# Kernel optimization log

Hardware: AMD Instinct MI355X
Metric: run time of the kernel (lower is better)

The kernel has to match this reference:

```python
import jax, jax.numpy as jnp
import numpy as np

D_MODEL = 2048
N_HEADS = 16
N_KV_HEADS = 4
HEAD_DIM = D_MODEL // N_HEADS  # 128
ROPE_BASE = 10000.0


def _rope_tables(T, head_dim):
    half = head_dim // 2
    theta = 1.0 / (ROPE_BASE ** (jnp.arange(half, dtype=jnp.float32) / half))
    m = jnp.arange(T, dtype=jnp.float32)
    freqs = jnp.outer(m, theta)  # (T, half)
    return jnp.cos(freqs), jnp.sin(freqs)


def _apply_rope(x, cos, sin):
    # x: (B, H, T, hd); rotate first/second halves as pairs
    half = x.shape[-1] // 2
    x1, x2 = x[..., :half], x[..., half:]
    cos = cos[None, None, :, :]
    sin = sin[None, None, :, :]
    return jnp.concatenate([x1 * cos - x2 * sin, x1 * sin + x2 * cos], axis=-1)


def setup_inputs() -> dict:
    key = jax.random.key(0)
    ks = jax.random.split(key, 5)
    B, T = 4, 2048
    x = jax.random.normal(ks[0], (B, T, D_MODEL), dtype=jnp.float32)
    Wq = jax.random.normal(ks[1], (D_MODEL, N_HEADS * HEAD_DIM), dtype=jnp.float32) * 0.02
    Wk = jax.random.normal(ks[2], (D_MODEL, N_KV_HEADS * HEAD_DIM), dtype=jnp.float32) * 0.02
    Wv = jax.random.normal(ks[3], (D_MODEL, N_KV_HEADS * HEAD_DIM), dtype=jnp.float32) * 0.02
    Wo = jax.random.normal(ks[4], (N_HEADS * HEAD_DIM, D_MODEL), dtype=jnp.float32) * (0.02 / np.sqrt(2.0))
    return {"x": x, "Wq": Wq, "Wk": Wk, "Wv": Wv, "Wo": Wo}


def reference(x, Wq, Wk, Wv, Wo):
    B, T, C = x.shape
    groups = N_HEADS // N_KV_HEADS

    # QKV projections
    q = (x @ Wq).reshape(B, T, N_HEADS, HEAD_DIM).transpose(0, 2, 1, 3)      # (B,H,T,hd)
    k = (x @ Wk).reshape(B, T, N_KV_HEADS, HEAD_DIM).transpose(0, 2, 1, 3)   # (B,Hkv,T,hd)
    v = (x @ Wv).reshape(B, T, N_KV_HEADS, HEAD_DIM).transpose(0, 2, 1, 3)

    # RoPE on q and k
    cos, sin = _rope_tables(T, HEAD_DIM)
    q = _apply_rope(q, cos, sin)
    k = _apply_rope(k, cos, sin)

    # GQA: repeat each kv head `groups` times
    k = jnp.repeat(k, groups, axis=1)  # (B,H,T,hd)
    v = jnp.repeat(v, groups, axis=1)

    # Attention scores with ALiBi bias and causal mask
    scale = 1.0 / np.sqrt(HEAD_DIM)
    scores = jnp.einsum('bhqd,bhkd->bhqk', q, k) * scale  # (B,H,T,T)

    pos = jnp.arange(T)
    dist = jnp.minimum(pos[None, :] - pos[:, None], 0).astype(jnp.float32)  # (T,T), <=0
    slopes = 2.0 ** (-8.0 * jnp.arange(1, N_HEADS + 1, dtype=jnp.float32) / N_HEADS)
    alibi = slopes[:, None, None] * dist[None, :, :]  # (H,T,T)
    scores = scores + alibi[None]

    causal = pos[None, :] > pos[:, None]  # True = future = blocked
    scores = jnp.where(causal[None, None], -jnp.inf, scores)

    weights = jax.nn.softmax(scores, axis=-1)
    out = jnp.einsum('bhqk,bhkd->bhqd', weights, v)  # (B,H,T,hd)
    out = out.transpose(0, 2, 1, 3).reshape(B, T, N_HEADS * HEAD_DIM)
    return out @ Wo
```

## Files before the change

### kernel.cpp

```cpp
#include <hip/hip_runtime.h>
#include <hip/hip_bf16.h>
#include <stdint.h>

#define T_SEQ 2048
#define DM    2048
#define NH    16
#define NKVH  4
#define HD    128
#define NBATCH 4
#define BT    (NBATCH * T_SEQ)
#define ATT_SCALE 0.08838834764831845f
#define LOG2E 1.4426950408889634f

typedef __attribute__((ext_vector_type(8))) short bf16x8;
typedef __attribute__((ext_vector_type(4))) float f32x4;
typedef __attribute__((ext_vector_type(16))) float f32x16;
typedef __attribute__((ext_vector_type(8))) unsigned short ushort8;
typedef __attribute__((ext_vector_type(4))) unsigned short ushort4v;

static __device__ __forceinline__ unsigned short f2bf(float f) {
  __hip_bfloat16 h = __float2bfloat16(f);
  return __builtin_bit_cast(unsigned short, h);
}
static __device__ __forceinline__ float bf2f(unsigned short u) {
  unsigned int v = ((unsigned int)u) << 16;
  return __builtin_bit_cast(float, v);
}
static __device__ __forceinline__ unsigned int packbf2(float a, float b) {
  return (unsigned int)f2bf(a) | ((unsigned int)f2bf(b) << 16);
}

#define GLDS16(g, l)                                                        \
  __builtin_amdgcn_global_load_lds(                                         \
      (const __attribute__((address_space(1))) void*)(g),                   \
      (__attribute__((address_space(3))) void*)(l), 16, 0, 0)

__global__ __launch_bounds__(256) void castx_k(const float* __restrict__ x,
                                               unsigned short* __restrict__ xb) {
  int i = (blockIdx.x * 256 + threadIdx.x) * 4;
  float4 v = *(const float4*)&x[i];
  ushort4v o;
  o[0] = f2bf(v.x); o[1] = f2bf(v.y); o[2] = f2bf(v.z); o[3] = f2bf(v.w);
  *(ushort4v*)&xb[i] = o;
}

__global__ __launch_bounds__(256) void transw_k(const float* __restrict__ src,
                                                unsigned short* __restrict__ dst,
                                                int ncols) {
  __shared__ unsigned short t[64][72];
  int n0 = blockIdx.x * 64, r0 = blockIdx.y * 64;
  int tid = threadIdx.x;
  int tx = tid & 15, ty = tid >> 4;
#pragma unroll
  for (int i = 0; i < 4; i++) {
    int r = ty * 4 + i;
    float4 v = *(const float4*)&src[(size_t)(r0 + r) * ncols + n0 + tx * 4];
    t[r][tx * 4 + 0] = f2bf(v.x);
    t[r][tx * 4 + 1] = f2bf(v.y);
    t[r][tx * 4 + 2] = f2bf(v.z);
    t[r][tx * 4 + 3] = f2bf(v.w);
  }
  __syncthreads();
  int nl = tid >> 2, seg = tid & 3;
  ushort8 o0, o1;
#pragma unroll
  for (int j = 0; j < 8; j++) {
    o0[j] = t[seg * 16 + j][nl];
    o1[j] = t[seg * 16 + 8 + j][nl];
  }
  size_t base = (size_t)(n0 + nl) * 2048 + r0 + seg * 16;
  *(ushort8*)&dst[base] = o0;
  *(ushort8*)&dst[base + 8] = o1;
}

template <int EPI>
__global__ __launch_bounds__(256) void gemm_k(const unsigned short* __restrict__ A,
                                              const unsigned short* __restrict__ Bt,
                                              unsigned short* __restrict__ q_out,
                                              unsigned short* __restrict__ k_out,
                                              unsigned short* __restrict__ v_out,
                                              float* __restrict__ f_out) {
  __shared__ unsigned short As[128 * 32];
  __shared__ unsigned short Bs[128 * 32];
  const int tid = threadIdx.x;
  const int lane = tid & 63;
  const int wid = tid >> 6;
  const int wr = wid >> 1, wc = wid & 1;
  const int row0 = blockIdx.x * 128, n00 = blockIdx.y * 128;
  const int lr = lane & 15, lk = (lane >> 4) * 8;
  const int c0 = tid, c1 = tid + 256;

  f32x4 acc[4][4] = {};

  for (int k0 = 0; k0 < 2048; k0 += 32) {
    __syncthreads();
    GLDS16(A + (size_t)(row0 + (c0 >> 2)) * 2048 + k0 + (c0 & 3) * 8, &As[c0 * 8]);
    GLDS16(A + (size_t)(row0 + (c1 >> 2)) * 2048 + k0 + (c1 & 3) * 8, &As[c1 * 8]);
    GLDS16(Bt + (size_t)(n00 + (c0 >> 2)) * 2048 + k0 + (c0 & 3) * 8, &Bs[c0 * 8]);
    GLDS16(Bt + (size_t)(n00 + (c1 >> 2)) * 2048 + k0 + (c1 & 3) * 8, &Bs[c1 * 8]);
    __syncthreads();
    bf16x8 af[4], bfr[4];
#pragma unroll
    for (int mi = 0; mi < 4; mi++)
      af[mi] = *(const bf16x8*)&As[(wr * 64 + mi * 16 + lr) * 32 + lk];
#pragma unroll
    for (int ni = 0; ni < 4; ni++)
      bfr[ni] = *(const bf16x8*)&Bs[(wc * 64 + ni * 16 + lr) * 32 + lk];
#pragma unroll
    for (int mi = 0; mi < 4; mi++)
#pragma unroll
      for (int ni = 0; ni < 4; ni++)
        acc[mi][ni] =
            __builtin_amdgcn_mfma_f32_16x16x32_bf16(af[mi], bfr[ni], acc[mi][ni], 0, 0, 0);
  }

  const int rbase = row0 + wr * 64;
  const int cbase = n00 + wc * 64;
#pragma unroll
  for (int mi = 0; mi < 4; mi++)
#pragma unroll
    for (int ni = 0; ni < 4; ni++)
#pragma unroll
      for (int r = 0; r < 4; r++) {
        int row = rbase + mi * 16 + (lane >> 4) * 4 + r;
        int col = cbase + ni * 16 + lr;
        float v = acc[mi][ni][r];
        if (EPI == 0) {
          if (col < 2048) {
            q_out[(size_t)row * 2048 + col] = f2bf(v);
          } else if (col < 2560) {
            k_out[(size_t)row * 512 + (col - 2048)] = f2bf(v);
          } else {
            int nv = col - 2560;
            int kvh = nv >> 7, d = nv & 127;
            int b = row >> 11, tt = row & 2047;
            v_out[((size_t)(b * NKVH + kvh) * HD + d) * T_SEQ + tt] = f2bf(v);
          }
        } else {
          f_out[(size_t)row * 2048 + col] = v;
        }
      }
}

__global__ __launch_bounds__(256) void rope_k(unsigned short* __restrict__ qb,
                                              unsigned short* __restrict__ kb) {
  int idx = blockIdx.x * 256 + threadIdx.x;
  int i = idx & 63;
  int wi = idx >> 6;
  int hh = wi % (NH + NKVH);
  int bt = wi / (NH + NKVH);
  int t = bt & (T_SEQ - 1);
  unsigned short* p = (hh < NH) ? (qb + (size_t)bt * 2048 + hh * HD)
                                : (kb + (size_t)bt * 512 + (hh - NH) * HD);
  float theta = exp2f(-(float)i * (13.287712379549449f / 64.0f));
  float ang = (float)t * theta;
  float s, c;
  sincosf(ang, &s, &c);
  float x1 = bf2f(p[i]), x2 = bf2f(p[i + 64]);
  p[i] = f2bf(x1 * c - x2 * s);
  p[i + 64] = f2bf(x1 * s + x2 * c);
}

__global__ __launch_bounds__(256) void attn_k(const unsigned short* __restrict__ qb,
                                              const unsigned short* __restrict__ kb,
                                              const unsigned short* __restrict__ vt,
                                              unsigned short* __restrict__ ao) {
  __shared__ __align__(16) unsigned short smem[17408];

  const int bid = blockIdx.x;
  const int level = bid >> 6;
  const int j = 15 - level;
  const int rr = bid & 63;
  const int s8 = rr & 7;
  const int w8 = rr >> 3;
  const int g = s8 + 8 * (w8 & 1);
  const int hh = w8 >> 1;
  const int b = g >> 2, kvh = g & 3;
  const int h = kvh * 4 + hh;

  const int tid = threadIdx.x;
  const int wid = tid >> 6, lane = tid & 63;
  const int l31 = lane & 31, lh = lane >> 5;
  const float slope2 = exp2f(-0.5f * (float)(h + 1)) * LOG2E;
  const float scale2 = ATT_SCALE * LOG2E;

  const int q0 = j * 128 + wid * 32;
  const int dt_w = j * 4 + wid;
  const int T_blk = j * 4 + 4;

  const int krow = tid >> 4;
  const int kchunk = tid & 15;
  const int cgk = kchunk ^ (krow & 7);
  const int vrow = tid >> 2;
  const int vchunk = tid & 3;
  const int cgv = vchunk ^ (vrow & 3);
  const int kxor = l31 & 7;
  const int vxor = l31 & 3;

  const unsigned short* khead = kb + (size_t)(b * T_SEQ) * 512 + kvh * 128;
  const unsigned short* vhead = vt + (size_t)(b * NKVH + kvh) * HD * T_SEQ;

  auto stage = [&](int buf, int k0) {
#pragma unroll
    for (int c = 0; c < 2; c++)
      GLDS16(khead + (size_t)(k0 + c * 16 + krow) * 512 + cgk * 8,
             &smem[buf * 4096 + c * 2048 + tid * 8]);
#pragma unroll
    for (int c = 0; c < 2; c++)
      GLDS16(vhead + (size_t)(c * 64 + vrow) * T_SEQ + k0 + cgv * 8,
             &smem[8192 + buf * 4096 + c * 2048 + tid * 8]);
  };

  unsigned short (*ot)[32][136] = (unsigned short(*)[32][136])smem;

  const unsigned short* qrow =
      qb + ((size_t)(b * T_SEQ + q0 + l31)) * 2048 + h * HD + lh * 8;
  bf16x8 qf[8];
#pragma unroll
  for (int ds = 0; ds < 8; ds++) qf[ds] = *(const bf16x8*)&qrow[ds * 16];

  f32x16 oacc[4] = {};
  float m2 = -1e30f, l_sum = 0.f;
  const float arow = -slope2 * (float)(q0 + l31);

  stage(0, 32 * (T_blk - 1));
  __syncthreads();
  int cur = 0;

#pragma unroll 1
  for (int it = 0; it < T_blk; ++it) {
    const int tt = T_blk - 1 - it;
    if (it + 1 < T_blk) stage(cur ^ 1, 32 * (tt - 1));

    if (tt <= dt_w) {
      const int k0 = tt * 32;
      const unsigned short* Kb = &smem[cur * 4096];
      const unsigned short* Vb = &smem[8192 + cur * 4096];

      bf16x8 kf[8];
#pragma unroll
      for (int ds = 0; ds < 8; ds++)
        kf[ds] = *(const bf16x8*)&Kb[l31 * 128 + ((2 * ds + lh) ^ kxor) * 8];

      __builtin_amdgcn_s_setprio(1);
      f32x16 sca = 0.f, scb = 0.f;
#pragma unroll
      for (int ds = 0; ds < 4; ds++)
        sca = __builtin_amdgcn_mfma_f32_32x32x16_bf16(kf[ds], qf[ds], sca, 0, 0, 0);
#pragma unroll
      for (int ds = 4; ds < 8; ds++)
        scb = __builtin_amdgcn_mfma_f32_32x32x16_bf16(kf[ds], qf[ds], scb, 0, 0, 0);
      __builtin_amdgcn_s_setprio(0);

      bf16x8 vf[4][2];
#pragma unroll
      for (int dt = 0; dt < 4; dt++)
#pragma unroll
        for (int ks = 0; ks < 2; ks++)
          vf[dt][ks] =
              *(const bf16x8*)&Vb[(dt * 32 + l31) * 32 + ((2 * ks + lh) ^ vxor) * 8];

      float s[16];
      const float ab = fmaf(slope2, (float)k0, arow);
      const bool diag = (tt == dt_w);
#pragma unroll
      for (int r = 0; r < 16; r++) {
        const int crow = (r & 3) + 8 * (r >> 2) + 4 * lh;
        float v = fmaf(sca[r] + scb[r], scale2, fmaf(slope2, (float)crow, ab));
        if (diag && crow > l31) v = -1e30f;
        s[r] = v;
      }

      float t8[8], t4[4];
#pragma unroll
      for (int i = 0; i < 8; i++) t8[i] = fmaxf(s[i], s[i + 8]);
#pragma unroll
      for (int i = 0; i < 4; i++) t4[i] = fmaxf(t8[i], t8[i + 4]);
      float mx = fmaxf(fmaxf(t4[0], t4[1]), fmaxf(t4[2], t4[3]));
      mx = fmaxf(mx, __shfl_xor(mx, 32));

      if (__any(mx > m2 + 8.f)) {
        const float mnew = fmaxf(m2, mx);
        const float corr = exp2f(m2 - mnew);
        l_sum *= corr;
#pragma unroll
        for (int dt = 0; dt < 4; dt++) oacc[dt] *= corr;
        m2 = mnew;
      }

      float pr[16];
#pragma unroll
      for (int r = 0; r < 16; r++) pr[r] = exp2f(s[r] - m2);

      float a8[8], a4[4];
#pragma unroll
      for (int i = 0; i < 8; i++) a8[i] = pr[i] + pr[i + 8];
#pragma unroll
      for (int i = 0; i < 4; i++) a4[i] = a8[i] + a8[i + 4];
      float rs = (a4[0] + a4[1]) + (a4[2] + a4[3]);
      rs += __shfl_xor(rs, 32);
      l_sum += rs;

      unsigned int w[8];
#pragma unroll
      for (int i = 0; i < 8; i++) w[i] = packbf2(pr[2 * i], pr[2 * i + 1]);
      const unsigned int ta = __shfl_xor(lh ? w[0] : w[2], 32);
      const unsigned int tb = __shfl_xor(lh ? w[1] : w[3], 32);
      const unsigned int tc = __shfl_xor(lh ? w[4] : w[6], 32);
      const unsigned int td = __shfl_xor(lh ? w[5] : w[7], 32);
      union U4 { unsigned int u[4]; bf16x8 v; } f0, f1;
      f0.u[0] = lh ? ta : w[0];
      f0.u[1] = lh ? tb : w[1];
      f0.u[2] = lh ? w[2] : ta;
      f0.u[3] = lh ? w[3] : tb;
      f1.u[0] = lh ? tc : w[4];
      f1.u[1] = lh ? td : w[5];
      f1.u[2] = lh ? w[6] : tc;
      f1.u[3] = lh ? w[7] : td;

      __builtin_amdgcn_s_setprio(1);
#pragma unroll
      for (int dt = 0; dt < 4; dt++) {
        oacc[dt] =
            __builtin_amdgcn_mfma_f32_32x32x16_bf16(vf[dt][0], f0.v, oacc[dt], 0, 0, 0);
        oacc[dt] =
            __builtin_amdgcn_mfma_f32_32x32x16_bf16(vf[dt][1], f1.v, oacc[dt], 0, 0, 0);
      }
      __builtin_amdgcn_s_setprio(0);
    }

    __syncthreads();
    cur ^= 1;
  }

  const float inv = 1.0f / l_sum;
#pragma unroll
  for (int dt = 0; dt < 4; dt++)
#pragma unroll
    for (int rg = 0; rg < 4; rg++) {
      ushort4v o;
#pragma unroll
      for (int jj = 0; jj < 4; jj++) o[jj] = f2bf(oacc[dt][rg * 4 + jj] * inv);
      *(ushort4v*)&ot[wid][l31][dt * 32 + rg * 8 + lh * 4] = o;
    }
  __syncthreads();
  const int rrow = lane >> 4, chunk = lane & 15;
#pragma unroll
  for (int ps = 0; ps < 8; ps++) {
    const int row = ps * 4 + rrow;
    ushort8 v = *(const ushort8*)&ot[wid][row][chunk * 8];
    *(ushort8*)&ao[((size_t)(b * T_SEQ + q0 + row)) * 2048 + h * HD + chunk * 8] = v;
  }
}

extern "C" void kernel_launch(void* const* d_in, const int* in_sizes, int n_in,
                              void* d_out, int out_size, void* d_ws, size_t ws_size,
                              hipStream_t stream) {
  const float* x = (const float*)d_in[0];
  const float* Wq = (const float*)d_in[1];
  const float* Wk = (const float*)d_in[2];
  const float* Wv = (const float*)d_in[3];
  const float* Wo = (const float*)d_in[4];

  char* w = (char*)d_ws;
  unsigned short* xb = (unsigned short*)w;
  unsigned short* wqt = (unsigned short*)(w + 33554432);
  unsigned short* qb = (unsigned short*)(w + 33554432 + 12582912);
  unsigned short* kb = (unsigned short*)(w + 33554432 + 12582912 + 33554432);
  unsigned short* vtb = (unsigned short*)(w + 33554432 + 12582912 + 33554432 + 8388608);

  castx_k<<<16384, 256, 0, stream>>>(x, xb);
  transw_k<<<dim3(32, 32), 256, 0, stream>>>(Wq, wqt, 2048);
  transw_k<<<dim3(8, 32), 256, 0, stream>>>(Wk, wqt + (size_t)2048 * 2048, 512);
  transw_k<<<dim3(8, 32), 256, 0, stream>>>(Wv, wqt + (size_t)2560 * 2048, 512);
  gemm_k<0><<<dim3(64, 24), 256, 0, stream>>>(xb, wqt, qb, kb, vtb, nullptr);
  rope_k<<<40960, 256, 0, stream>>>(qb, kb);
  transw_k<<<dim3(32, 32), 256, 0, stream>>>(Wo, wqt, 2048);
  attn_k<<<1024, 256, 0, stream>>>(qb, kb, vtb, xb);
  gemm_k<1><<<dim3(64, 16), 256, 0, stream>>>(xb, wqt, nullptr, nullptr, nullptr,
                                              (float*)d_out);
}
```

Measured before the change: 486.7 us.

## Pair causal query tiles per block and stage 64-key tiles in attention

Each attention block now handles two query tiles, j and 15-j, one after the other, so every block does the same causal work. The grid drops from 1024 to 512 blocks. K/V staging moves from 32-key to 64-key tiles, which doubles shared memory to 64KB and halves the number of barrier iterations. This targets load imbalance and the tail from the causal triangle. In exchange it lowers occupancy, since larger LDS per block may allow fewer resident blocks, and it serializes the two halves within each block.

```diff
diff --git a/kernel.cpp b/kernel.cpp
--- a/kernel.cpp
+++ b/kernel.cpp
@@ -165,16 +165,14 @@
                                               const unsigned short* __restrict__ kb,
                                               const unsigned short* __restrict__ vt,
                                               unsigned short* __restrict__ ao) {
-  __shared__ __align__(16) unsigned short smem[17408];
+  __shared__ __align__(16) unsigned short smem[32768];
 
   const int bid = blockIdx.x;
-  const int level = bid >> 6;
-  const int j = 15 - level;
-  const int rr = bid & 63;
-  const int s8 = rr & 7;
-  const int w8 = rr >> 3;
-  const int g = s8 + 8 * (w8 & 1);
-  const int hh = w8 >> 1;
+  const int s8 = bid & 7;
+  const int rest = bid >> 3;
+  const int p = rest & 7;
+  const int hh = (rest >> 3) & 3;
+  const int g = s8 + 8 * (rest >> 5);
   const int b = g >> 2, kvh = g & 3;
   const int h = kvh * 4 + hh;
 
@@ -184,172 +182,176 @@
   const float slope2 = exp2f(-0.5f * (float)(h + 1)) * LOG2E;
   const float scale2 = ATT_SCALE * LOG2E;
 
-  const int q0 = j * 128 + wid * 32;
-  const int dt_w = j * 4 + wid;
-  const int T_blk = j * 4 + 4;
-
   const int krow = tid >> 4;
-  const int kchunk = tid & 15;
-  const int cgk = kchunk ^ (krow & 7);
-  const int vrow = tid >> 2;
-  const int vchunk = tid & 3;
-  const int cgv = vchunk ^ (vrow & 3);
-  const int kxor = l31 & 7;
-  const int vxor = l31 & 3;
+  const int cgk = (tid & 15) ^ (krow & 7);
+  const int vrow7 = (tid >> 3) & 7;
+  const int cgv = (tid & 7) ^ vrow7;
+  const int xr = l31 & 7;
 
   const unsigned short* khead = kb + (size_t)(b * T_SEQ) * 512 + kvh * 128;
   const unsigned short* vhead = vt + (size_t)(b * NKVH + kvh) * HD * T_SEQ;
 
   auto stage = [&](int buf, int k0) {
 #pragma unroll
-    for (int c = 0; c < 2; c++)
+    for (int c = 0; c < 4; c++)
       GLDS16(khead + (size_t)(k0 + c * 16 + krow) * 512 + cgk * 8,
-             &smem[buf * 4096 + c * 2048 + tid * 8]);
-#pragma unroll
-    for (int c = 0; c < 2; c++)
-      GLDS16(vhead + (size_t)(c * 64 + vrow) * T_SEQ + k0 + cgv * 8,
-             &smem[8192 + buf * 4096 + c * 2048 + tid * 8]);
+             &smem[buf * 8192 + c * 2048 + tid * 8]);
+#pragma unroll
+    for (int c = 0; c < 4; c++)
+      GLDS16(vhead + (size_t)(c * 32 + (tid >> 3)) * T_SEQ + k0 + cgv * 8,
+             &smem[16384 + buf * 8192 + c * 2048 + tid * 8]);
   };
 
   unsigned short (*ot)[32][136] = (unsigned short(*)[32][136])smem;
 
-  const unsigned short* qrow =
-      qb + ((size_t)(b * T_SEQ + q0 + l31)) * 2048 + h * HD + lh * 8;
-  bf16x8 qf[8];
-#pragma unroll
-  for (int ds = 0; ds < 8; ds++) qf[ds] = *(const bf16x8*)&qrow[ds * 16];
-
-  f32x16 oacc[4] = {};
-  float m2 = -1e30f, l_sum = 0.f;
-  const float arow = -slope2 * (float)(q0 + l31);
-
-  stage(0, 32 * (T_blk - 1));
-  __syncthreads();
-  int cur = 0;
-
 #pragma unroll 1
-  for (int it = 0; it < T_blk; ++it) {
-    const int tt = T_blk - 1 - it;
-    if (it + 1 < T_blk) stage(cur ^ 1, 32 * (tt - 1));
-
-    if (tt <= dt_w) {
-      const int k0 = tt * 32;
-      const unsigned short* Kb = &smem[cur * 4096];
-      const unsigned short* Vb = &smem[8192 + cur * 4096];
-
-      bf16x8 kf[8];
-#pragma unroll
-      for (int ds = 0; ds < 8; ds++)
-        kf[ds] = *(const bf16x8*)&Kb[l31 * 128 + ((2 * ds + lh) ^ kxor) * 8];
-
-      __builtin_amdgcn_s_setprio(1);
-      f32x16 sca = 0.f, scb = 0.f;
-#pragma unroll
-      for (int ds = 0; ds < 4; ds++)
-        sca = __builtin_amdgcn_mfma_f32_32x32x16_bf16(kf[ds], qf[ds], sca, 0, 0, 0);
-#pragma unroll
-      for (int ds = 4; ds < 8; ds++)
-        scb = __builtin_amdgcn_mfma_f32_32x32x16_bf16(kf[ds], qf[ds], scb, 0, 0, 0);
-      __builtin_amdgcn_s_setprio(0);
-
-      bf16x8 vf[4][2];
-#pragma unroll
-      for (int dt = 0; dt < 4; dt++)
-#pragma unroll
-        for (int ks = 0; ks < 2; ks++)
-          vf[dt][ks] =
-              *(const bf16x8*)&Vb[(dt * 32 + l31) * 32 + ((2 * ks + lh) ^ vxor) * 8];
-
-      float s[16];
-      const float ab = fmaf(slope2, (float)k0, arow);
-      const bool diag = (tt == dt_w);
-#pragma unroll
-      for (int r = 0; r < 16; r++) {
-        const int crow = (r & 3) + 8 * (r >> 2) + 4 * lh;
-        float v = fmaf(sca[r] + scb[r], scale2, fmaf(slope2, (float)crow, ab));
-        if (diag && crow > l31) v = -1e30f;
-        s[r] = v;
+  for (int half = 0; half < 2; ++half) {
+    const int j = half ? (15 - p) : p;
+    const int q0 = j * 128 + wid * 32;
+    const int dt32 = j * 4 + wid;
+    const int nt = 2 * j + 2;
+
+    const unsigned short* qrow =
+        qb + ((size_t)(b * T_SEQ + q0 + l31)) * 2048 + h * HD + lh * 8;
+    bf16x8 qf[8];
+#pragma unroll
+    for (int ds = 0; ds < 8; ds++) qf[ds] = *(const bf16x8*)&qrow[ds * 16];
+
+    f32x16 oacc[4] = {};
+    float m2 = -1e30f, l_sum = 0.f;
+    const float arow = -slope2 * (float)(q0 + l31);
+
+    __syncthreads();
+    stage(0, 64 * (nt - 1));
+    __syncthreads();
+    int cur = 0;
+
+#pragma unroll 1
+    for (int it = 0; it < nt; ++it) {
+      const int tt = nt - 1 - it;
+      if (it + 1 < nt) stage(cur ^ 1, 64 * (tt - 1));
+
+      const unsigned short* Kb = &smem[cur * 8192];
+      const unsigned short* Vb = &smem[16384 + cur * 8192];
+
+#pragma unroll
+      for (int ms = 1; ms >= 0; --ms) {
+        const int k32 = tt * 2 + ms;
+        if (k32 <= dt32) {
+          const int k0m = k32 * 32;
+
+          bf16x8 kf[8];
+#pragma unroll
+          for (int ds = 0; ds < 8; ds++)
+            kf[ds] = *(const bf16x8*)&Kb[(ms * 32 + l31) * 128 + ((2 * ds + lh) ^ xr) * 8];
+
+          __builtin_amdgcn_s_setprio(1);
+          f32x16 sc = 0.f;
+#pragma unroll
+          for (int ds = 0; ds < 8; ds++)
+            sc = __builtin_amdgcn_mfma_f32_32x32x16_bf16(kf[ds], qf[ds], sc, 0, 0, 0);
+          __builtin_amdgcn_s_setprio(0);
+
+          bf16x8 vf[4][2];
+#pragma unroll
+          for (int dt = 0; dt < 4; dt++)
+#pragma unroll
+            for (int ks = 0; ks < 2; ks++)
+              vf[dt][ks] = *(const bf16x8*)&Vb[(dt * 32 + l31) * 64 +
+                                               ((ms * 4 + 2 * ks + lh) ^ xr) * 8];
+
+          float s[16];
+          const float ab = fmaf(slope2, (float)k0m, arow);
+          const bool diag = (k32 == dt32);
+#pragma unroll
+          for (int r = 0; r < 16; r++) {
+            const int crow = (r & 3) + 8 * (r >> 2) + 4 * lh;
+            float v = fmaf(sc[r], scale2, fmaf(slope2, (float)crow, ab));
+            if (diag && crow > l31) v = -1e30f;
+            s[r] = v;
+          }
+
+          float t8[8], t4[4];
+#pragma unroll
+          for (int i = 0; i < 8; i++) t8[i] = fmaxf(s[i], s[i + 8]);
+#pragma unroll
+          for (int i = 0; i < 4; i++) t4[i] = fmaxf(t8[i], t8[i + 4]);
+          float mx = fmaxf(fmaxf(t4[0], t4[1]), fmaxf(t4[2], t4[3]));
+          mx = fmaxf(mx, __shfl_xor(mx, 32));
+
+          if (__any(mx > m2 + 8.f)) {
+            const float mnew = fmaxf(m2, mx);
+            const float corr = exp2f(m2 - mnew);
+            l_sum *= corr;
+#pragma unroll
+            for (int dt = 0; dt < 4; dt++) oacc[dt] *= corr;
+            m2 = mnew;
+          }
+
+          float pr[16];
+#pragma unroll
+          for (int r = 0; r < 16; r++) pr[r] = exp2f(s[r] - m2);
+
+          float a8[8], a4[4];
+#pragma unroll
+          for (int i = 0; i < 8; i++) a8[i] = pr[i] + pr[i + 8];
+#pragma unroll
+          for (int i = 0; i < 4; i++) a4[i] = a8[i] + a8[i + 4];
+          float rs = (a4[0] + a4[1]) + (a4[2] + a4[3]);
+          rs += __shfl_xor(rs, 32);
+          l_sum += rs;
+
+          unsigned int w[8];
+#pragma unroll
+          for (int i = 0; i < 8; i++) w[i] = packbf2(pr[2 * i], pr[2 * i + 1]);
+          const unsigned int ta = __shfl_xor(lh ? w[0] : w[2], 32);
+          const unsigned int tb = __shfl_xor(lh ? w[1] : w[3], 32);
+          const unsigned int tc = __shfl_xor(lh ? w[4] : w[6], 32);
+          const unsigned int td = __shfl_xor(lh ? w[5] : w[7], 32);
+          union U4 { unsigned int u[4]; bf16x8 v; } f0, f1;
+          f0.u[0] = lh ? ta : w[0];
+          f0.u[1] = lh ? tb : w[1];
+          f0.u[2] = lh ? w[2] : ta;
+          f0.u[3] = lh ? w[3] : tb;
+          f1.u[0] = lh ? tc : w[4];
+          f1.u[1] = lh ? td : w[5];
+          f1.u[2] = lh ? w[6] : tc;
+          f1.u[3] = lh ? w[7] : td;
+
+          __builtin_amdgcn_s_setprio(1);
+#pragma unroll
+          for (int dt = 0; dt < 4; dt++) {
+            oacc[dt] =
+                __builtin_amdgcn_mfma_f32_32x32x16_bf16(vf[dt][0], f0.v, oacc[dt], 0, 0, 0);
+            oacc[dt] =
+                __builtin_amdgcn_mfma_f32_32x32x16_bf16(vf[dt][1], f1.v, oacc[dt], 0, 0, 0);
+          }
+          __builtin_amdgcn_s_setprio(0);
+        }
       }
 
-      float t8[8], t4[4];
-#pragma unroll
-      for (int i = 0; i < 8; i++) t8[i] = fmaxf(s[i], s[i + 8]);
-#pragma unroll
-      for (int i = 0; i < 4; i++) t4[i] = fmaxf(t8[i], t8[i + 4]);
-      float mx = fmaxf(fmaxf(t4[0], t4[1]), fmaxf(t4[2], t4[3]));
-      mx = fmaxf(mx, __shfl_xor(mx, 32));
-
-      if (__any(mx > m2 + 8.f)) {
-        const float mnew = fmaxf(m2, mx);
-        const float corr = exp2f(m2 - mnew);
-        l_sum *= corr;
-#pragma unroll
-        for (int dt = 0; dt < 4; dt++) oacc[dt] *= corr;
-        m2 = mnew;
+      __syncthreads();
+      cur ^= 1;
+    }
+
+    const float inv = 1.0f / l_sum;
+#pragma unroll
+    for (int dt = 0; dt < 4; dt++)
+#pragma unroll
+      for (int rg = 0; rg < 4; rg++) {
+        ushort4v o;
+#pragma unroll
+        for (int jj = 0; jj < 4; jj++) o[jj] = f2bf(oacc[dt][rg * 4 + jj] * inv);
+        *(ushort4v*)&ot[wid][l31][dt * 32 + rg * 8 + lh * 4] = o;
       }
-
-      float pr[16];
-#pragma unroll
-      for (int r = 0; r < 16; r++) pr[r] = exp2f(s[r] - m2);
-
-      float a8[8], a4[4];
-#pragma unroll
-      for (int i = 0; i < 8; i++) a8[i] = pr[i] + pr[i + 8];
-#pragma unroll
-      for (int i = 0; i < 4; i++) a4[i] = a8[i] + a8[i + 4];
-      float rs = (a4[0] + a4[1]) + (a4[2] + a4[3]);
-      rs += __shfl_xor(rs, 32);
-      l_sum += rs;
-
-      unsigned int w[8];
-#pragma unroll
-      for (int i = 0; i < 8; i++) w[i] = packbf2(pr[2 * i], pr[2 * i + 1]);
-      const unsigned int ta = __shfl_xor(lh ? w[0] : w[2], 32);
-      const unsigned int tb = __shfl_xor(lh ? w[1] : w[3], 32);
-      const unsigned int tc = __shfl_xor(lh ? w[4] : w[6], 32);
-      const unsigned int td = __shfl_xor(lh ? w[5] : w[7], 32);
-      union U4 { unsigned int u[4]; bf16x8 v; } f0, f1;
-      f0.u[0] = lh ? ta : w[0];
-      f0.u[1] = lh ? tb : w[1];
-      f0.u[2] = lh ? w[2] : ta;
-      f0.u[3] = lh ? w[3] : tb;
-      f1.u[0] = lh ? tc : w[4];
-      f1.u[1] = lh ? td : w[5];
-      f1.u[2] = lh ? w[6] : tc;
-      f1.u[3] = lh ? w[7] : td;
-
-      __builtin_amdgcn_s_setprio(1);
-#pragma unroll
-      for (int dt = 0; dt < 4; dt++) {
-        oacc[dt] =
-            __builtin_amdgcn_mfma_f32_32x32x16_bf16(vf[dt][0], f0.v, oacc[dt], 0, 0, 0);
-        oacc[dt] =
-            __builtin_amdgcn_mfma_f32_32x32x16_bf16(vf[dt][1], f1.v, oacc[dt], 0, 0, 0);
-      }
-      __builtin_amdgcn_s_setprio(0);
+    __syncthreads();
+    const int rrow = lane >> 4, chunk = lane & 15;
+#pragma unroll
+    for (int ps = 0; ps < 8; ps++) {
+      const int row = ps * 4 + rrow;
+      ushort8 v = *(const ushort8*)&ot[wid][row][chunk * 8];
+      *(ushort8*)&ao[((size_t)(b * T_SEQ + q0 + row)) * 2048 + h * HD + chunk * 8] = v;
     }
-
-    __syncthreads();
-    cur ^= 1;
-  }
-
-  const float inv = 1.0f / l_sum;
-#pragma unroll
-  for (int dt = 0; dt < 4; dt++)
-#pragma unroll
-    for (int rg = 0; rg < 4; rg++) {
-      ushort4v o;
-#pragma unroll
-      for (int jj = 0; jj < 4; jj++) o[jj] = f2bf(oacc[dt][rg * 4 + jj] * inv);
-      *(ushort4v*)&ot[wid][l31][dt * 32 + rg * 8 + lh * 4] = o;
-    }
-  __syncthreads();
-  const int rrow = lane >> 4, chunk = lane & 15;
-#pragma unroll
-  for (int ps = 0; ps < 8; ps++) {
-    const int row = ps * 4 + rrow;
-    ushort8 v = *(const ushort8*)&ot[wid][row][chunk * 8];
-    *(ushort8*)&ao[((size_t)(b * T_SEQ + q0 + row)) * 2048 + h * HD + chunk * 8] = v;
   }
 }
 
@@ -376,7 +378,7 @@
   gemm_k<0><<<dim3(64, 24), 256, 0, stream>>>(xb, wqt, qb, kb, vtb, nullptr);
   rope_k<<<40960, 256, 0, stream>>>(qb, kb);
   transw_k<<<dim3(32, 32), 256, 0, stream>>>(Wo, wqt, 2048);
-  attn_k<<<1024, 256, 0, stream>>>(qb, kb, vtb, xb);
+  attn_k<<<512, 256, 0, stream>>>(qb, kb, vtb, xb);
   gemm_k<1><<<dim3(64, 16), 256, 0, stream>>>(xb, wqt, nullptr, nullptr, nullptr,
                                               (float*)d_out);
 }
```

After: 471.1 us. -3.2%, faster.
